# Performance work log

Hardware: AMD Instinct MI355X
Metric: run time of the kernel (lower is better)

## Reference

```python
import jax, jax.numpy as jnp
import numpy as np

B, T, E = 16, 1024, 1024
H, Dh = 16, 64


def setup_inputs() -> dict:
    key = jax.random.key(0)
    ks = jax.random.split(key, 6)
    s = 1.0 / np.sqrt(E)
    x = jax.random.normal(ks[0], (B, T, E), dtype=jnp.float32)
    Wq = jax.random.uniform(ks[1], (H, E, Dh), minval=-s, maxval=s, dtype=jnp.float32)
    Wk = jax.random.uniform(ks[2], (H, E, Dh), minval=-s, maxval=s, dtype=jnp.float32)
    Wv = jax.random.uniform(ks[3], (H, E, Dh), minval=-s, maxval=s, dtype=jnp.float32)
    sp = 1.0 / np.sqrt(H * Dh)
    Wo = jax.random.uniform(ks[4], (H * Dh, E), minval=-sp, maxval=sp, dtype=jnp.float32)
    bo = jax.random.uniform(ks[5], (E,), minval=-sp, maxval=sp, dtype=jnp.float32)
    return {"x": x, "Wq": Wq, "Wk": Wk, "Wv": Wv, "Wo": Wo, "bo": bo}


def reference(x, Wq, Wk, Wv, Wo, bo):
    # batched per-head projections: [B,T,E] x [H,E,Dh] -> [B,H,T,Dh]
    q = jnp.einsum('bte,hed->bhtd', x, Wq)
    k = jnp.einsum('bte,hed->bhtd', x, Wk)
    v = jnp.einsum('bte,hed->bhtd', x, Wv)
    scale = 1.0 / np.sqrt(Dh).astype(np.float32)
    wei = jnp.einsum('bhtd,bhsd->bhts', q, k) * scale  # [B,H,T,T]
    causal = jnp.tril(jnp.ones((T, T), dtype=bool))
    wei = jnp.where(causal, wei, -jnp.inf)
    wei = jax.nn.softmax(wei, axis=-1)
    out = jnp.einsum('bhts,bhsd->bhtd', wei, v)  # [B,H,T,Dh]
    out = out.transpose(0, 2, 1, 3).reshape(B, T, H * Dh)  # concat heads
    return out @ Wo + bo
```

## Files before the change

kernel.cpp:

```cpp
#include <hip/hip_runtime.h>
#include <stdint.h>

typedef __attribute__((ext_vector_type(8))) short short8;
typedef __attribute__((ext_vector_type(4))) float f32x4;
typedef __attribute__((ext_vector_type(4))) unsigned short u16x4;

#define DEVI static __device__ __forceinline__

DEVI unsigned short f2bf(float f) {
  unsigned int u = __builtin_bit_cast(unsigned int, f);
  u += 0x7fffu + ((u >> 16) & 1u);
  return (unsigned short)(u >> 16);
}

DEVI void glds16(const void* g, void* lds_uniform) {
  typedef const __attribute__((address_space(1))) unsigned int* gp_t;
  typedef __attribute__((address_space(3))) unsigned int* lp_t;
  __builtin_amdgcn_global_load_lds((gp_t)(uintptr_t)g, (lp_t)(uintptr_t)lds_uniform, 16, 0, 0);
}


__global__ __launch_bounds__(256) void cvt_x_kernel(const float* __restrict__ in,
                                                    unsigned short* __restrict__ out, int n4) {
  typedef __attribute__((ext_vector_type(4))) float f4;
  typedef __attribute__((ext_vector_type(4))) unsigned short u4;
  const f4* in4 = (const f4*)in;
  u4* out4 = (u4*)out;
  for (int i = blockIdx.x * blockDim.x + threadIdx.x; i < n4; i += gridDim.x * blockDim.x) {
    f4 v = in4[i];
    u4 o;
    o[0] = f2bf(v[0]); o[1] = f2bf(v[1]); o[2] = f2bf(v[2]); o[3] = f2bf(v[3]);
    out4[i] = o;
  }
}

__global__ __launch_bounds__(256) void cvt_w_kernel(const float* __restrict__ in,
                                                    unsigned short* __restrict__ out,
                                                    int total, int log2C) {
  int i = blockIdx.x * blockDim.x + threadIdx.x;
  if (i >= total) return;
  int r = i & 1023;
  int rest = i >> 10;
  int c = rest & ((1 << log2C) - 1);
  int b = rest >> log2C;
  out[i] = f2bf(in[((((size_t)b << 10) | (size_t)r) << log2C) | (size_t)c]);
}

template <int MODE>
__global__ __launch_bounds__(256)
void gemm128(const unsigned short* __restrict__ A,
             const unsigned short* __restrict__ Bt,
             unsigned short* __restrict__ OutB,
             float* __restrict__ OutF,
             const float* __restrict__ bias) {
  __shared__ unsigned short As[128 * 64];
  __shared__ unsigned short Bs[128 * 64];
  const int tid = threadIdx.x;
  const int w = tid >> 6, lane = tid & 63;
  const int l15 = lane & 15, l4 = lane >> 4;
  const int bm = blockIdx.y << 7, bn = blockIdx.x << 7;
  const unsigned short* Bz = Bt + (size_t)blockIdx.z * (1024 * 1024);

  f32x4 acc[4][4];
#pragma unroll
  for (int i = 0; i < 4; ++i)
#pragma unroll
    for (int j = 0; j < 4; ++j) acc[i][j] = f32x4{0.f, 0.f, 0.f, 0.f};

  const int wr = w >> 1, wc = w & 1;

  int Crow[4], Kel[4];
#pragma unroll
  for (int j = 0; j < 4; ++j) {
    int C = (((j << 2) + w) << 6) + lane;
    int row = C >> 3, cc = C & 7;
    Crow[j] = row;
    Kel[j] = ((cc ^ (row & 7)) << 3);
  }

  for (int kt = 0; kt < 16; ++kt) {
    int k0 = kt << 6;
#pragma unroll
    for (int j = 0; j < 4; ++j) {
      const unsigned short* g = A + (size_t)(bm + Crow[j]) * 1024 + k0 + Kel[j];
      glds16(g, &As[(size_t)(((j << 2) + w) << 6) * 8]);
    }
#pragma unroll
    for (int j = 0; j < 4; ++j) {
      const unsigned short* g = Bz + (size_t)(bn + Crow[j]) * 1024 + k0 + Kel[j];
      glds16(g, &Bs[(size_t)(((j << 2) + w) << 6) * 8]);
    }
    __syncthreads();
#pragma unroll
    for (int ks = 0; ks < 2; ++ks) {
      short8 af[4], bfr[4];
#pragma unroll
      for (int mi = 0; mi < 4; ++mi) {
        int row = (wr << 6) + (mi << 4) + l15;
        int ch = ((ks << 2) + l4) ^ (row & 7);
        af[mi] = *(const short8*)&As[(row << 6) + (ch << 3)];
      }
#pragma unroll
      for (int ni = 0; ni < 4; ++ni) {
        int row = (wc << 6) + (ni << 4) + l15;
        int ch = ((ks << 2) + l4) ^ (row & 7);
        bfr[ni] = *(const short8*)&Bs[(row << 6) + (ch << 3)];
      }
#pragma unroll
      for (int mi = 0; mi < 4; ++mi)
#pragma unroll
        for (int ni = 0; ni < 4; ++ni)
          acc[mi][ni] = __builtin_amdgcn_mfma_f32_16x16x32_bf16(af[mi], bfr[ni], acc[mi][ni], 0, 0, 0);
    }
    __syncthreads();
  }

  if (MODE == 0) {
    if (blockIdx.z < 2) {
      unsigned short* Oz = OutB + (size_t)blockIdx.z * 16777216;
#pragma unroll
      for (int mi = 0; mi < 4; ++mi) {
#pragma unroll
        for (int r = 0; r < 4; ++r) {
          int m = bm + (wr << 6) + (mi << 4) + (l4 << 2) + r;
          int b = m >> 10, t = m & 1023;
#pragma unroll
          for (int ni = 0; ni < 4; ++ni) {
            int n = bn + (wc << 6) + (ni << 4) + l15;
            int h = n >> 6, d = n & 63;
            Oz[((size_t)(b * 16 + h) * 1024 + t) * 64 + d] = f2bf(acc[mi][ni][r]);
          }
        }
      }
    } else {
      unsigned short* Oz = OutB + (size_t)2 * 16777216;
#pragma unroll
      for (int mi = 0; mi < 4; ++mi) {
        int tb = bm + (wr << 6) + (mi << 4) + (l4 << 2);
        int bb = tb >> 10, tt = tb & 1023;
#pragma unroll
        for (int ni = 0; ni < 4; ++ni) {
          int n = bn + (wc << 6) + (ni << 4) + l15;
          int hh = n >> 6, dd = n & 63;
          u16x4 pk;
#pragma unroll
          for (int r = 0; r < 4; ++r) pk[r] = f2bf(acc[mi][ni][r]);
          *(u16x4*)&Oz[(((size_t)((bb << 4) + hh) << 6) + (size_t)dd) * 1024 + tt] = pk;
        }
      }
    }
  } else {
#pragma unroll
    for (int mi = 0; mi < 4; ++mi) {
#pragma unroll
      for (int r = 0; r < 4; ++r) {
        int m = bm + (wr << 6) + (mi << 4) + (l4 << 2) + r;
#pragma unroll
        for (int ni = 0; ni < 4; ++ni) {
          int n = bn + (wc << 6) + (ni << 4) + l15;
          OutF[(size_t)m * 1024 + n] = acc[mi][ni][r] + bias[n];
        }
      }
    }
  }
}

__global__ __launch_bounds__(256)
void attn_fa(const unsigned short* __restrict__ Qb,
             const unsigned short* __restrict__ Kb,
             const unsigned short* __restrict__ Vtb,
             unsigned short* __restrict__ Ob) {
  __shared__ unsigned short Ks[2][64 * 64];
  __shared__ unsigned short Vs[2][64 * 64];
  __shared__ unsigned short Ps[4][16 * 64];
  const int tid = threadIdx.x, w = tid >> 6, lane = tid & 63;
  const int l15 = lane & 15, l4 = lane >> 4;
  const int bx = blockIdx.x, bh = blockIdx.y;
  const unsigned short* Q = Qb + ((size_t)bh << 16);
  const unsigned short* K = Kb + ((size_t)bh << 16);
  const unsigned short* Vt = Vtb + ((size_t)bh << 16);
  const int b = bh >> 4, h = bh & 15;
  const float SC = 0.125f * 1.44269504088896340736f;
  const float NEGINF = -__builtin_inff();

  int srow[2], skoff[2];
#pragma unroll
  for (int c = 0; c < 2; ++c) {
    int C = (c << 8) + tid;
    int row = C >> 3, cc = C & 7;
    srow[c] = row;
    skoff[c] = ((cc ^ (row & 7)) << 3);
  }
  const int sdst = (w << 6) << 3;

  for (int ph = 0; ph < 2; ++ph) {
    const int qidx = ph ? bx : (15 - bx);
    const int q0 = qidx << 6;
    const int nt = qidx + 1;
    const int qrow = q0 + (w << 4) + l15;

    short8 bq0, bq1;
    {
      const unsigned short* qp = Q + (size_t)qrow * 64 + (l4 << 3);
      bq0 = *(const short8*)qp;
      bq1 = *(const short8*)(qp + 32);
    }

    f32x4 o[4];
#pragma unroll
    for (int nf = 0; nf < 4; ++nf) o[nf] = f32x4{0.f, 0.f, 0.f, 0.f};
    float mreg = NEGINF, lreg = 0.f;

#pragma unroll
    for (int c = 0; c < 2; ++c) {
      glds16(K + (size_t)(srow[c] << 6) + skoff[c], &Ks[0][(c << 11) + sdst]);
      glds16(Vt + (size_t)(srow[c] << 10) + skoff[c], &Vs[0][(c << 11) + sdst]);
    }
    __syncthreads();

    for (int it = 0; it < nt; ++it) {
      const int cur = it & 1;
      if (it + 1 < nt) {
        const int kv0n = (it + 1) << 6;
#pragma unroll
        for (int c = 0; c < 2; ++c) {
          glds16(K + (size_t)((kv0n + srow[c]) << 6) + skoff[c], &Ks[cur ^ 1][(c << 11) + sdst]);
          glds16(Vt + (size_t)(srow[c] << 10) + kv0n + skoff[c], &Vs[cur ^ 1][(c << 11) + sdst]);
        }
      }

      f32x4 s[4];
#pragma unroll
      for (int n = 0; n < 4; ++n) {
        const int row = (n << 4) + l15;
        const int rb = row << 6;
        short8 ak0 = *(const short8*)&Ks[cur][rb + ((l4 ^ (row & 7)) << 3)];
        short8 ak1 = *(const short8*)&Ks[cur][rb + (((4 + l4) ^ (row & 7)) << 3)];
        f32x4 a = f32x4{0.f, 0.f, 0.f, 0.f};
        a = __builtin_amdgcn_mfma_f32_16x16x32_bf16(ak0, bq0, a, 0, 0, 0);
        a = __builtin_amdgcn_mfma_f32_16x16x32_bf16(ak1, bq1, a, 0, 0, 0);
        s[n] = a;
      }

      const int kv0 = it << 6;
      const bool diag = (it == nt - 1);
      float p[4][4];
      float mx = NEGINF;
#pragma unroll
      for (int n = 0; n < 4; ++n)
#pragma unroll
        for (int r = 0; r < 4; ++r) {
          float v = s[n][r] * SC;
          if (diag) {
            int kvg = kv0 + (n << 4) + (l4 << 2) + r;
            v = (kvg <= qrow) ? v : NEGINF;
          }
          p[n][r] = v;
          mx = fmaxf(mx, v);
        }
      mx = fmaxf(mx, __shfl_xor(mx, 16));
      mx = fmaxf(mx, __shfl_xor(mx, 32));
      float mnew = fmaxf(mreg, mx);
      float alpha = exp2f(mreg - mnew);
      mreg = mnew;
      float rs = 0.f;
#pragma unroll
      for (int n = 0; n < 4; ++n)
#pragma unroll
        for (int r = 0; r < 4; ++r) {
          float pv = exp2f(p[n][r] - mreg);
          p[n][r] = pv;
          rs += pv;
        }
      rs += __shfl_xor(rs, 16);
      rs += __shfl_xor(rs, 32);
      lreg = lreg * alpha + rs;

      float a_r[4];
#pragma unroll
      for (int r = 0; r < 4; ++r)
        a_r[r] = __shfl(alpha, (lane & 0x30) | ((l4 << 2) | r));
#pragma unroll
      for (int nf = 0; nf < 4; ++nf)
#pragma unroll
        for (int r = 0; r < 4; ++r) o[nf][r] *= a_r[r];

#pragma unroll
      for (int n = 0; n < 4; ++n) {
        u16x4 pk;
#pragma unroll
        for (int r = 0; r < 4; ++r) pk[r] = f2bf(p[n][r]);
        const int kc = (n << 1) + (l4 >> 1);
        char* addr = (char*)&Ps[w][0] + (l15 << 7) + ((kc ^ (l15 & 7)) << 4) + ((l4 & 1) << 3);
        *(u16x4*)addr = pk;
      }

      short8 pa0 = *(const short8*)((char*)&Ps[w][0] + (l15 << 7) + ((l4 ^ (l15 & 7)) << 4));
      short8 pa1 = *(const short8*)((char*)&Ps[w][0] + (l15 << 7) + (((4 + l4) ^ (l15 & 7)) << 4));
#pragma unroll
      for (int nf = 0; nf < 4; ++nf) {
        const int drow = (nf << 4) + l15;
        const int db = drow << 6;
        short8 vb0 = *(const short8*)&Vs[cur][db + ((l4 ^ (drow & 7)) << 3)];
        short8 vb1 = *(const short8*)&Vs[cur][db + (((4 + l4) ^ (drow & 7)) << 3)];
        o[nf] = __builtin_amdgcn_mfma_f32_16x16x32_bf16(pa0, vb0, o[nf], 0, 0, 0);
        o[nf] = __builtin_amdgcn_mfma_f32_16x16x32_bf16(pa1, vb1, o[nf], 0, 0, 0);
      }
      __syncthreads();
    }

    float linv = 1.0f / lreg;
    float l_r[4];
#pragma unroll
    for (int r = 0; r < 4; ++r)
      l_r[r] = __shfl(linv, (lane & 0x30) | ((l4 << 2) | r));
#pragma unroll
    for (int r = 0; r < 4; ++r) {
      const int t = q0 + (w << 4) + (l4 << 2) + r;
      size_t base = ((size_t)(b * 1024 + t) << 10) + (h << 6);
#pragma unroll
      for (int nf = 0; nf < 4; ++nf)
        Ob[base + (nf << 4) + l15] = f2bf(o[nf][r] * l_r[r]);
    }
    __syncthreads();
  }
}


extern "C" void kernel_launch(void* const* d_in, const int* in_sizes, int n_in,
                              void* d_out, int out_size, void* d_ws, size_t ws_size,
                              hipStream_t stream) {
  const float* x  = (const float*)d_in[0];
  const float* Wq = (const float*)d_in[1];
  const float* Wk = (const float*)d_in[2];
  const float* Wv = (const float*)d_in[3];
  const float* Wo = (const float*)d_in[4];
  const float* bo = (const float*)d_in[5];
  float* out = (float*)d_out;

  unsigned char* ws = (unsigned char*)d_ws;
  unsigned short* xb  = (unsigned short*)(ws);
  unsigned short* wT  = (unsigned short*)(ws + 33554432);
  unsigned short* woT = (unsigned short*)(ws + 33554432 + 6291456);
  unsigned short* qkv = (unsigned short*)(ws + 41943040);
  unsigned short* Ob  = xb;

  cvt_x_kernel<<<2048, 256, 0, stream>>>(x, xb, 4194304);
  cvt_w_kernel<<<4096, 256, 0, stream>>>(Wq, wT,              1 << 20, 6);
  cvt_w_kernel<<<4096, 256, 0, stream>>>(Wk, wT + (1 << 20),  1 << 20, 6);
  cvt_w_kernel<<<4096, 256, 0, stream>>>(Wv, wT + (2 << 20),  1 << 20, 6);
  cvt_w_kernel<<<4096, 256, 0, stream>>>(Wo, woT,             1 << 20, 10);

  gemm128<0><<<dim3(8, 128, 3), 256, 0, stream>>>(xb, wT, qkv, nullptr, nullptr);
  attn_fa<<<dim3(8, 256), 256, 0, stream>>>(qkv, qkv + 16777216, qkv + 33554432, Ob);
  gemm128<1><<<dim3(8, 128, 1), 256, 0, stream>>>(Ob, woT, nullptr, out, bo);
}
```

Baseline: 452.8 us.

## Remap workgroups for XCD-aware L2 locality and raise MFMA wave priority

```diff
diff --git a/kernel.cpp b/kernel.cpp
--- a/kernel.cpp
+++ b/kernel.cpp
@@ -58,8 +58,15 @@
   const int tid = threadIdx.x;
   const int w = tid >> 6, lane = tid & 63;
   const int l15 = lane & 15, l4 = lane >> 4;
-  const int bm = blockIdx.y << 7, bn = blockIdx.x << 7;
-  const unsigned short* Bz = Bt + (size_t)blockIdx.z * (1024 * 1024);
+
+  const int SN = (MODE == 0) ? 6 : 2;
+  const int q8 = (MODE == 0) ? 384 : 128;
+  const int phys = blockIdx.x;
+  const int wgid = (phys & 7) * q8 + (phys >> 3);
+  const int st = wgid >> 4, loc = wgid & 15;
+  const int sm = st / SN, sn = st % SN;
+  const int bm = (((sm << 2) + (loc >> 2)) << 7);
+  const int bn = (((sn << 2) + (loc & 3)) << 7);
 
   f32x4 acc[4][4];
 #pragma unroll
@@ -87,10 +94,11 @@
     }
 #pragma unroll
     for (int j = 0; j < 4; ++j) {
-      const unsigned short* g = Bz + (size_t)(bn + Crow[j]) * 1024 + k0 + Kel[j];
+      const unsigned short* g = Bt + (size_t)(bn + Crow[j]) * 1024 + k0 + Kel[j];
       glds16(g, &Bs[(size_t)(((j << 2) + w) << 6) * 8]);
     }
     __syncthreads();
+    __builtin_amdgcn_s_setprio(1);
 #pragma unroll
     for (int ks = 0; ks < 2; ++ks) {
       short8 af[4], bfr[4];
@@ -112,12 +120,15 @@
         for (int ni = 0; ni < 4; ++ni)
           acc[mi][ni] = __builtin_amdgcn_mfma_f32_16x16x32_bf16(af[mi], bfr[ni], acc[mi][ni], 0, 0, 0);
     }
+    __builtin_amdgcn_s_setprio(0);
     __syncthreads();
   }
 
   if (MODE == 0) {
-    if (blockIdx.z < 2) {
-      unsigned short* Oz = OutB + (size_t)blockIdx.z * 16777216;
+    const int nb = bn + (wc << 6);
+    const int z = nb >> 10;
+    if (z < 2) {
+      unsigned short* Oz = OutB + (size_t)z * 16777216;
 #pragma unroll
       for (int mi = 0; mi < 4; ++mi) {
 #pragma unroll
@@ -126,8 +137,8 @@
           int b = m >> 10, t = m & 1023;
 #pragma unroll
           for (int ni = 0; ni < 4; ++ni) {
-            int n = bn + (wc << 6) + (ni << 4) + l15;
-            int h = n >> 6, d = n & 63;
+            int n1 = (nb + (ni << 4) + l15) & 1023;
+            int h = n1 >> 6, d = n1 & 63;
             Oz[((size_t)(b * 16 + h) * 1024 + t) * 64 + d] = f2bf(acc[mi][ni][r]);
           }
         }
@@ -140,8 +151,8 @@
         int bb = tb >> 10, tt = tb & 1023;
 #pragma unroll
         for (int ni = 0; ni < 4; ++ni) {
-          int n = bn + (wc << 6) + (ni << 4) + l15;
-          int hh = n >> 6, dd = n & 63;
+          int n1 = (nb + (ni << 4) + l15) & 1023;
+          int hh = n1 >> 6, dd = n1 & 63;
           u16x4 pk;
 #pragma unroll
           for (int r = 0; r < 4; ++r) pk[r] = f2bf(acc[mi][ni][r]);
@@ -175,7 +186,10 @@
   __shared__ unsigned short Ps[4][16 * 64];
   const int tid = threadIdx.x, w = tid >> 6, lane = tid & 63;
   const int l15 = lane & 15, l4 = lane >> 4;
-  const int bx = blockIdx.x, bh = blockIdx.y;
+  const int phys = blockIdx.x;
+  const int ord = phys >> 3;
+  const int bx = ord & 7;
+  const int bh = ((phys & 7) << 5) | (ord >> 3);
   const unsigned short* Q = Qb + ((size_t)bh << 16);
   const unsigned short* K = Kb + ((size_t)bh << 16);
   const unsigned short* Vt = Vtb + ((size_t)bh << 16);
@@ -230,6 +244,7 @@
       }
 
       f32x4 s[4];
+      __builtin_amdgcn_s_setprio(1);
 #pragma unroll
       for (int n = 0; n < 4; ++n) {
         const int row = (n << 4) + l15;
@@ -241,6 +256,7 @@
         a = __builtin_amdgcn_mfma_f32_16x16x32_bf16(ak1, bq1, a, 0, 0, 0);
         s[n] = a;
       }
+      __builtin_amdgcn_s_setprio(0);
 
       const int kv0 = it << 6;
       const bool diag = (it == nt - 1);
@@ -297,6 +313,7 @@
 
       short8 pa0 = *(const short8*)((char*)&Ps[w][0] + (l15 << 7) + ((l4 ^ (l15 & 7)) << 4));
       short8 pa1 = *(const short8*)((char*)&Ps[w][0] + (l15 << 7) + (((4 + l4) ^ (l15 & 7)) << 4));
+      __builtin_amdgcn_s_setprio(1);
 #pragma unroll
       for (int nf = 0; nf < 4; ++nf) {
         const int drow = (nf << 4) + l15;
@@ -306,6 +323,7 @@
         o[nf] = __builtin_amdgcn_mfma_f32_16x16x32_bf16(pa0, vb0, o[nf], 0, 0, 0);
         o[nf] = __builtin_amdgcn_mfma_f32_16x16x32_bf16(pa1, vb1, o[nf], 0, 0, 0);
       }
+      __builtin_amdgcn_s_setprio(0);
       __syncthreads();
     }
 
@@ -322,7 +340,6 @@
       for (int nf = 0; nf < 4; ++nf)
         Ob[base + (nf << 4) + l15] = f2bf(o[nf][r] * l_r[r]);
     }
-    __syncthreads();
   }
 }
 
@@ -351,7 +368,7 @@
   cvt_w_kernel<<<4096, 256, 0, stream>>>(Wv, wT + (2 << 20),  1 << 20, 6);
   cvt_w_kernel<<<4096, 256, 0, stream>>>(Wo, woT,             1 << 20, 10);
 
-  gemm128<0><<<dim3(8, 128, 3), 256, 0, stream>>>(xb, wT, qkv, nullptr, nullptr);
-  attn_fa<<<dim3(8, 256), 256, 0, stream>>>(qkv, qkv + 16777216, qkv + 33554432, Ob);
-  gemm128<1><<<dim3(8, 128, 1), 256, 0, stream>>>(Ob, woT, nullptr, out, bo);
-}
+  gemm128<0><<<3072, 256, 0, stream>>>(xb, wT, qkv, nullptr, nullptr);
+  attn_fa<<<2048, 256, 0, stream>>>(qkv, qkv + 16777216, qkv + 33554432, Ob);
+  gemm128<1><<<1024, 256, 0, stream>>>(Ob, woT, nullptr, out, bo);
+}
```

Result: faster. 418.9 us (-7.5%).
